# Optimization experiments

Hardware: AMD Instinct MI355X
Metric: run time of the kernel (lower is better)

## Reference

```python
import jax, jax.numpy as jnp
import numpy as np

SEQ = 8192
DIM = 1280
NHEADS = 16
HEAD_DIM = DIM // NHEADS  # 80
NSEG = 8
SEG = SEQ // NSEG  # 1024


def setup_inputs() -> dict:
    key = jax.random.key(0)
    ks = jax.random.split(key, 7)
    hidden_states = jax.random.normal(ks[0], (SEQ, DIM), jnp.float32)
    # realistic rotary embeddings: cos/sin of random angles, shape [S, head_dim]
    ang = jax.random.uniform(ks[1], (SEQ, HEAD_DIM), jnp.float32, 0.0, 2.0 * np.pi)
    cos = jnp.cos(ang)
    sin = jnp.sin(ang)
    qkv_w = jax.random.normal(ks[2], (3 * DIM, DIM), jnp.float32) * (DIM ** -0.5)
    qkv_b = jax.random.normal(ks[3], (3 * DIM,), jnp.float32) * 0.02
    proj_w = jax.random.normal(ks[4], (DIM, DIM), jnp.float32) * (DIM ** -0.5)
    proj_b = jax.random.normal(ks[5], (DIM,), jnp.float32) * 0.02
    cu_seqlens = jnp.arange(NSEG + 1, dtype=jnp.int32) * SEG  # equal segments
    return {"hidden_states": hidden_states, "cos": cos, "sin": sin,
            "qkv_w": qkv_w, "qkv_b": qkv_b, "proj_w": proj_w, "proj_b": proj_b,
            "cu_seqlens": cu_seqlens}


def _rope(x, cos, sin):
    # x: [S, H, D]; cos/sin: [S, D] broadcast over heads. Computed in fp32.
    x = x.astype(jnp.float32)
    d = x.shape[-1]
    x1, x2 = x[..., : d // 2], x[..., d // 2:]
    rot = jnp.concatenate([-x2, x1], axis=-1)
    return x * cos[:, None, :] + rot * sin[:, None, :]


def reference(hidden_states, cos, sin, qkv_w, qkv_b, proj_w, proj_b, cu_seqlens):
    S, dim = hidden_states.shape
    nseg = cu_seqlens.shape[0] - 1
    seg = S // nseg  # segments are equal-length; block-diagonal attention batches over them
    H, D = NHEADS, dim // NHEADS

    qkv = hidden_states @ qkv_w.T + qkv_b                 # [S, 3*dim]
    qkv = qkv.reshape(S, 3, H, D)
    q, k, v = qkv[:, 0], qkv[:, 1], qkv[:, 2]             # [S, H, D]

    in_dtype = hidden_states.dtype
    q = _rope(q, cos, sin).astype(in_dtype)
    k = _rope(k, cos, sin).astype(in_dtype)

    scale = D ** -0.5
    qs = q.reshape(nseg, seg, H, D)
    ks = k.reshape(nseg, seg, H, D)
    vs = v.reshape(nseg, seg, H, D)

    scores = jnp.einsum('bqhd,bkhd->bhqk', qs, ks) * scale  # [nseg, H, seg, seg]
    probs = jax.nn.softmax(scores, axis=-1)
    out = jnp.einsum('bhqk,bkhd->bqhd', probs, vs)          # [nseg, seg, H, D]
    out = out.reshape(S, H * D)
    return out @ proj_w.T + proj_b
```

## Files before the change

kernel.cpp:

```cpp
#include <hip/hip_runtime.h>

#define SEQ 8192
#define DIM 1280
#define NHEADS 16
#define HD 80
#define HDP 96
#define NSEG 8
#define SEG 1024
#define KVB 64
#define NSTEP (SEG / KVB)
#define PST 72

typedef float f32x4 __attribute__((ext_vector_type(4)));
typedef short bf16x8 __attribute__((ext_vector_type(8)));
typedef unsigned int u32;

__device__ __forceinline__ float fast_exp2(float x) {
  return __builtin_amdgcn_exp2f(x);
}

__device__ __forceinline__ short f2bf(float f) {
  unsigned int u = __builtin_bit_cast(unsigned int, f);
  u = (u + 0x7fff + ((u >> 16) & 1)) >> 16;
  return (short)u;
}

__device__ __forceinline__ u32 cvt_pk_bf16(float lo, float hi) {
  u32 r;
  asm("v_cvt_pk_bf16_f32 %0, %1, %2" : "=v"(r) : "v"(lo), "v"(hi));
  return r;
}

typedef __attribute__((address_space(1))) const unsigned int glds_src_t;
typedef __attribute__((address_space(3))) unsigned int glds_dst_t;
__device__ __forceinline__ void gload_lds16(const void* g, void* l) {
  __builtin_amdgcn_global_load_lds((glds_src_t*)g, (glds_dst_t*)l, 16, 0, 0);
}

__global__ void cast_f32_bf16(const float* __restrict__ in, short* __restrict__ out, int n) {
  int n4 = n >> 2;
  for (int i = blockIdx.x * blockDim.x + threadIdx.x; i < n4; i += gridDim.x * blockDim.x) {
    float4 v = ((const float4*)in)[i];
    short4 o;
    o.x = f2bf(v.x); o.y = f2bf(v.y); o.z = f2bf(v.z); o.w = f2bf(v.w);
    ((short4*)out)[i] = o;
  }
}

__global__ __launch_bounds__(256) void gemm_bt_bias(
    const short* __restrict__ A, const short* __restrict__ B,
    const float* __restrict__ bias, float* __restrict__ C,
    int M, int N, int K) {
  __shared__ short As[128 * 64];
  __shared__ short Bs[128 * 64];
  int tid = threadIdx.x;
  int w = tid >> 6, l = tid & 63;
  int lrow = l & 15, lg = l >> 4;
  int bid = blockIdx.x;
  int cpx = gridDim.x >> 3;
  int lid = (bid & 7) * cpx + (bid >> 3);
  int ntx = N >> 7;
  int m0 = (lid / ntx) * 128, n0 = (lid % ntx) * 128;
  int wm = w & 1, wn = w >> 1;

  f32x4 acc[4][4] = {};

  const char* Abase = (const char*)A + (size_t)m0 * K * 2;
  const char* Bbase = (const char*)B + (size_t)n0 * K * 2;

  for (int k0 = 0; k0 < K; k0 += 64) {
#pragma unroll
    for (int j = 0; j < 4; j++) {
      int c = j * 256 + tid;
      int row = c >> 3;
      int sc = c & 7;
      int slc = sc ^ (row & 7);
      size_t goff = (size_t)row * K * 2 + (size_t)k0 * 2 + slc * 16;
      int loff = (j * 256 + w * 64) * 16;
      gload_lds16(Abase + goff, (char*)As + loff);
      gload_lds16(Bbase + goff, (char*)Bs + loff);
    }
    __syncthreads();
#pragma unroll
    for (int kk = 0; kk < 2; kk++) {
      bf16x8 a[4], b[4];
#pragma unroll
      for (int mt = 0; mt < 4; mt++) {
        int row = wm * 64 + mt * 16 + lrow;
        int p = (kk * 4 + lg) ^ (row & 7);
        a[mt] = *(const bf16x8*)&As[row * 64 + p * 8];
      }
#pragma unroll
      for (int nt = 0; nt < 4; nt++) {
        int row = wn * 64 + nt * 16 + lrow;
        int p = (kk * 4 + lg) ^ (row & 7);
        b[nt] = *(const bf16x8*)&Bs[row * 64 + p * 8];
      }
#pragma unroll
      for (int mt = 0; mt < 4; mt++)
#pragma unroll
        for (int nt = 0; nt < 4; nt++)
          acc[mt][nt] = __builtin_amdgcn_mfma_f32_16x16x32_bf16(a[mt], b[nt], acc[mt][nt], 0, 0, 0);
    }
    __syncthreads();
  }
#pragma unroll
  for (int nt = 0; nt < 4; nt++) {
    int col = n0 + wn * 64 + nt * 16 + lrow;
    float bv = bias[col];
#pragma unroll
    for (int mt = 0; mt < 4; mt++) {
      int mrow = m0 + wm * 64 + mt * 16 + lg * 4;
#pragma unroll
      for (int r = 0; r < 4; r++)
        C[(size_t)(mrow + r) * N + col] = acc[mt][nt][r] + bv;
    }
  }
}

__global__ void rope_qk(const float* __restrict__ qkv, const float* __restrict__ cosb,
                        const float* __restrict__ sinb, short* __restrict__ qg,
                        short* __restrict__ kg) {
  int t = blockIdx.x * blockDim.x + threadIdx.x;
  if (t >= SEQ * NHEADS * 40) return;
  int d = t % 40;
  int h = (t / 40) & 15;
  int s = t / 640;
  const float* row = qkv + (size_t)s * (3 * DIM);
  float c0 = cosb[s * HD + d], c1 = cosb[s * HD + d + 40];
  float s0 = sinb[s * HD + d], s1 = sinb[s * HD + d + 40];
  float x1 = row[h * HD + d], x2 = row[h * HD + d + 40];
  float q0 = x1 * c0 - x2 * s0;
  float q1 = x2 * c1 + x1 * s1;
  float y1 = row[DIM + h * HD + d], y2 = row[DIM + h * HD + d + 40];
  float k0 = y1 * c0 - y2 * s0;
  float k1 = y2 * c1 + y1 * s1;
  const float sc = 0.11180339887498949f * 1.4426950408889634f;
  size_t base = ((size_t)h * SEQ + s) * HDP;
  qg[base + d] = f2bf(q0 * sc);
  qg[base + d + 40] = f2bf(q1 * sc);
  kg[base + d] = f2bf(k0);
  kg[base + d + 40] = f2bf(k1);
  if (d < 16) { qg[base + 80 + d] = 0; kg[base + 80 + d] = 0; }
}

__global__ void v_transpose(const float* __restrict__ qkv, short* __restrict__ vt) {
  __shared__ float T[16][68];
  int st = blockIdx.x, dt = blockIdx.y, h = blockIdx.z;
  int d0 = dt * 16, s0 = st * 64;
  int t = threadIdx.x;
  int dd = t & 15, ss = t >> 4;
#pragma unroll
  for (int j = 0; j < 4; j++) {
    int s = ss + j * 16;
    T[dd][s] = qkv[(size_t)(s0 + s) * (3 * DIM) + 2 * DIM + h * HD + d0 + dd];
  }
  __syncthreads();
  int s2 = t & 63, dr = t >> 6;
#pragma unroll
  for (int j = 0; j < 4; j++) {
    int d = dr + j * 4;
    vt[((size_t)(h * HD + d0 + d)) * SEQ + s0 + s2] = f2bf(T[d][s2]);
  }
}

__global__ __launch_bounds__(512, 2) void attn_kernel(
    const short* __restrict__ qg, const short* __restrict__ kg,
    const short* __restrict__ vt, short* __restrict__ out) {
  __shared__ short Ks[2][64 * 128];
  __shared__ short Pl[8][32 * PST];
  int bid = blockIdx.x;
  int b = bid & 7, h = (bid >> 3) & 15, qt = bid >> 7;
  int tid = threadIdx.x;
  int w = tid >> 6, l = tid & 63;
  int lrow = l & 15, lg = l >> 4;
  int qbase_s = b * SEG + qt * 256 + w * 32;

  const short* qh = qg + (size_t)h * SEQ * HDP;
  const short* kh = kg + (size_t)h * SEQ * HDP;
  const short* vh = vt + (size_t)h * HD * SEQ;

#define STAGE_K(BUF, KEY0N)                                                    \
  {                                                                            \
    _Pragma("unroll") for (int sr = 0; sr < 2; sr++) {                         \
      int sbase = sr * 512 + w * 64;                                           \
      int ss = sbase + l;                                                      \
      int skey = ss >> 4, sc = ss & 15;                                        \
      int slc = sc ^ (skey & 7);                                               \
      const short* ssrc =                                                      \
          kh + (size_t)((KEY0N) + skey) * HDP + (slc < 12 ? slc * 8 : 0);      \
      gload_lds16(ssrc, (char*)&Ks[BUF][0] + sbase * 16);                      \
    }                                                                          \
  }

  bf16x8 qf[2][3];
#pragma unroll
  for (int mt = 0; mt < 2; mt++)
#pragma unroll
    for (int ks = 0; ks < 3; ks++)
      qf[mt][ks] = *(const bf16x8*)&qh[(size_t)(qbase_s + mt * 16 + lrow) * HDP + ks * 32 + lg * 8];

  f32x4 o[2][5] = {};
  float m_st[2] = {-1e30f, -1e30f};
  float l_st[2] = {0.f, 0.f};

  short* Pw = &Pl[w][0];

  STAGE_K(0, b * SEG);
  __syncthreads();

  for (int i = 0; i < NSTEP; i++) {
    int cur = i & 1;
    int key0 = b * SEG + i * KVB;
    if (i + 1 < NSTEP) {
      STAGE_K(cur ^ 1, key0 + KVB);
    }

    f32x4 sv[2][4] = {};
    __builtin_amdgcn_s_setprio(1);
#pragma unroll
    for (int kt = 0; kt < 4; kt++) {
      bf16x8 kf[3];
      int key = kt * 16 + lrow;
#pragma unroll
      for (int ks = 0; ks < 3; ks++) {
        int p = (ks * 4 + lg) ^ (key & 7);
        kf[ks] = *(const bf16x8*)&Ks[cur][key * 128 + p * 8];
      }
#pragma unroll
      for (int mt = 0; mt < 2; mt++)
#pragma unroll
        for (int ks = 0; ks < 3; ks++)
          sv[mt][kt] = __builtin_amdgcn_mfma_f32_16x16x32_bf16(kf[ks], qf[mt][ks], sv[mt][kt], 0, 0, 0);
    }
    __builtin_amdgcn_s_setprio(0);

    bf16x8 vf[5][2];
#pragma unroll
    for (int nt = 0; nt < 5; nt++)
#pragma unroll
      for (int ks = 0; ks < 2; ks++)
        vf[nt][ks] = *(const bf16x8*)&vh[(size_t)(nt * 16 + lrow) * SEQ + key0 + ks * 32 + lg * 8];

    float cm[2];
#pragma unroll
    for (int mt = 0; mt < 2; mt++) {
      float a0 = fmaxf(fmaxf(sv[mt][0][0], sv[mt][0][1]), fmaxf(sv[mt][0][2], sv[mt][0][3]));
      float a1 = fmaxf(fmaxf(sv[mt][1][0], sv[mt][1][1]), fmaxf(sv[mt][1][2], sv[mt][1][3]));
      float a2 = fmaxf(fmaxf(sv[mt][2][0], sv[mt][2][1]), fmaxf(sv[mt][2][2], sv[mt][2][3]));
      float a3 = fmaxf(fmaxf(sv[mt][3][0], sv[mt][3][1]), fmaxf(sv[mt][3][2], sv[mt][3][3]));
      float c = fmaxf(fmaxf(a0, a1), fmaxf(a2, a3));
      c = fmaxf(c, __shfl_xor(c, 16));
      c = fmaxf(c, __shfl_xor(c, 32));
      cm[mt] = c;
    }
    if (__any((cm[0] > m_st[0] + 8.f) || (cm[1] > m_st[1] + 8.f))) {
#pragma unroll
      for (int mt = 0; mt < 2; mt++) {
        float mn = fmaxf(m_st[mt], cm[mt]);
        float c = fast_exp2(m_st[mt] - mn);
        m_st[mt] = mn;
        l_st[mt] *= c;
        float cr[4];
#pragma unroll
        for (int r = 0; r < 4; r++) cr[r] = __shfl(c, lg * 4 + r);
#pragma unroll
        for (int nt = 0; nt < 5; nt++)
#pragma unroll
          for (int r = 0; r < 4; r++) o[mt][nt][r] *= cr[r];
      }
    }
#pragma unroll
    for (int mt = 0; mt < 2; mt++) {
      float rs = 0.f;
#pragma unroll
      for (int kt = 0; kt < 4; kt++) {
#pragma unroll
        for (int r = 0; r < 4; r++) {
          sv[mt][kt][r] = fast_exp2(sv[mt][kt][r] - m_st[mt]);
          rs += sv[mt][kt][r];
        }
        uint2 pk;
        pk.x = cvt_pk_bf16(sv[mt][kt][0], sv[mt][kt][1]);
        pk.y = cvt_pk_bf16(sv[mt][kt][2], sv[mt][kt][3]);
        *(uint2*)&Pw[(mt * 16 + lrow) * PST + kt * 16 + lg * 4] = pk;
      }
      rs += __shfl_xor(rs, 16);
      rs += __shfl_xor(rs, 32);
      l_st[mt] += rs;
    }

    bf16x8 pa[2][2];
#pragma unroll
    for (int mt = 0; mt < 2; mt++)
#pragma unroll
      for (int ks = 0; ks < 2; ks++)
        pa[mt][ks] = *(const bf16x8*)&Pw[(mt * 16 + lrow) * PST + ks * 32 + lg * 8];
    __builtin_amdgcn_s_setprio(1);
#pragma unroll
    for (int nt = 0; nt < 5; nt++)
#pragma unroll
      for (int mt = 0; mt < 2; mt++)
#pragma unroll
        for (int ks = 0; ks < 2; ks++)
          o[mt][nt] = __builtin_amdgcn_mfma_f32_16x16x32_bf16(pa[mt][ks], vf[nt][ks], o[mt][nt], 0, 0, 0);
    __builtin_amdgcn_s_setprio(0);

    __syncthreads();
  }

#pragma unroll
  for (int mt = 0; mt < 2; mt++) {
    float rl = 1.f / l_st[mt];
    float ir[4];
#pragma unroll
    for (int r = 0; r < 4; r++) ir[r] = __shfl(rl, lg * 4 + r);
#pragma unroll
    for (int r = 0; r < 4; r++) {
      int srow = qbase_s + mt * 16 + lg * 4 + r;
#pragma unroll
      for (int nt = 0; nt < 5; nt++)
        out[(size_t)srow * DIM + h * HD + nt * 16 + lrow] = f2bf(o[mt][nt][r] * ir[r]);
    }
  }
}

extern "C" void kernel_launch(void* const* d_in, const int* in_sizes, int n_in,
                              void* d_out, int out_size, void* d_ws, size_t ws_size,
                              hipStream_t stream) {
  const float* hidden = (const float*)d_in[0];
  const float* cosb = (const float*)d_in[1];
  const float* sinb = (const float*)d_in[2];
  const float* qkv_w = (const float*)d_in[3];
  const float* qkv_b = (const float*)d_in[4];
  const float* proj_w = (const float*)d_in[5];
  const float* proj_b = (const float*)d_in[6];

  char* ws = (char*)d_ws;
  float* qkv_f = (float*)(ws);
  short* attn_o = (short*)(ws);
  short* wp_bf = (short*)(ws + 23068672);
  short* q_bf = (short*)(ws + 125829120);
  short* k_bf = (short*)(ws + 150994944);
  short* v_tb = (short*)(ws + 176160768);
  short* h_bf = (short*)(ws + 197132288);
  short* wq_bf = (short*)(ws + 218103808);

  cast_f32_bf16<<<4096, 256, 0, stream>>>(hidden, h_bf, SEQ * DIM);
  cast_f32_bf16<<<4096, 256, 0, stream>>>(qkv_w, wq_bf, 3 * DIM * DIM);
  gemm_bt_bias<<<1920, 256, 0, stream>>>(h_bf, wq_bf, qkv_b, qkv_f, SEQ, 3 * DIM, DIM);
  rope_qk<<<20480, 256, 0, stream>>>(qkv_f, cosb, sinb, q_bf, k_bf);
  v_transpose<<<dim3(128, 5, 16), 256, 0, stream>>>(qkv_f, v_tb);
  cast_f32_bf16<<<2048, 256, 0, stream>>>(proj_w, wp_bf, DIM * DIM);
  attn_kernel<<<512, 512, 0, stream>>>(q_bf, k_bf, v_tb, attn_o);
  gemm_bt_bias<<<640, 256, 0, stream>>>(attn_o, wp_bf, proj_b, (float*)d_out, SEQ, DIM, DIM);
}
```

Baseline: 348.7 us.

## Emit bf16 QKV from GEMM and double-buffer GEMM LDS tiles

```diff
diff --git a/kernel.cpp b/kernel.cpp
--- a/kernel.cpp
+++ b/kernel.cpp
@@ -25,6 +25,11 @@
   return (short)u;
 }
 
+__device__ __forceinline__ float bf2f(short s) {
+  u32 u = ((u32)(unsigned short)s) << 16;
+  return __builtin_bit_cast(float, u);
+}
+
 __device__ __forceinline__ u32 cvt_pk_bf16(float lo, float hi) {
   u32 r;
   asm("v_cvt_pk_bf16_f32 %0, %1, %2" : "=v"(r) : "v"(lo), "v"(hi));
@@ -50,9 +55,9 @@
 __global__ __launch_bounds__(256) void gemm_bt_bias(
     const short* __restrict__ A, const short* __restrict__ B,
     const float* __restrict__ bias, float* __restrict__ C,
-    int M, int N, int K) {
-  __shared__ short As[128 * 64];
-  __shared__ short Bs[128 * 64];
+    short* __restrict__ Cb, int M, int N, int K) {
+  __shared__ short As[2][128 * 32];
+  __shared__ short Bs[2][128 * 32];
   int tid = threadIdx.x;
   int w = tid >> 6, l = tid & 63;
   int lrow = l & 15, lg = l >> 4;
@@ -68,42 +73,48 @@
   const char* Abase = (const char*)A + (size_t)m0 * K * 2;
   const char* Bbase = (const char*)B + (size_t)n0 * K * 2;
 
-  for (int k0 = 0; k0 < K; k0 += 64) {
-#pragma unroll
-    for (int j = 0; j < 4; j++) {
-      int c = j * 256 + tid;
-      int row = c >> 3;
-      int sc = c & 7;
-      int slc = sc ^ (row & 7);
-      size_t goff = (size_t)row * K * 2 + (size_t)k0 * 2 + slc * 16;
-      int loff = (j * 256 + w * 64) * 16;
-      gload_lds16(Abase + goff, (char*)As + loff);
-      gload_lds16(Bbase + goff, (char*)Bs + loff);
-    }
+#define STAGE_G(BUF, K0)                                                       \
+  {                                                                            \
+    _Pragma("unroll") for (int j = 0; j < 2; j++) {                            \
+      int c = j * 256 + tid;                                                   \
+      int row = c >> 2;                                                        \
+      int slc = (c & 3) ^ ((row >> 1) & 3);                                    \
+      size_t goff = (size_t)row * K * 2 + (size_t)(K0) * 2 + slc * 16;         \
+      int loff = (j * 256 + w * 64) * 16;                                      \
+      gload_lds16(Abase + goff, (char*)&As[BUF][0] + loff);                    \
+      gload_lds16(Bbase + goff, (char*)&Bs[BUF][0] + loff);                    \
+    }                                                                          \
+  }
+
+  STAGE_G(0, 0);
+  __syncthreads();
+
+  for (int k0 = 0; k0 < K; k0 += 32) {
+    int cur = (k0 >> 5) & 1;
+    if (k0 + 32 < K) {
+      STAGE_G(cur ^ 1, k0 + 32);
+    }
+    bf16x8 a[4], b[4];
+#pragma unroll
+    for (int mt = 0; mt < 4; mt++) {
+      int row = wm * 64 + mt * 16 + lrow;
+      int p = lg ^ ((row >> 1) & 3);
+      a[mt] = *(const bf16x8*)&As[cur][row * 32 + p * 8];
+    }
+#pragma unroll
+    for (int nt = 0; nt < 4; nt++) {
+      int row = wn * 64 + nt * 16 + lrow;
+      int p = lg ^ ((row >> 1) & 3);
+      b[nt] = *(const bf16x8*)&Bs[cur][row * 32 + p * 8];
+    }
+#pragma unroll
+    for (int mt = 0; mt < 4; mt++)
+#pragma unroll
+      for (int nt = 0; nt < 4; nt++)
+        acc[mt][nt] = __builtin_amdgcn_mfma_f32_16x16x32_bf16(a[mt], b[nt], acc[mt][nt], 0, 0, 0);
     __syncthreads();
-#pragma unroll
-    for (int kk = 0; kk < 2; kk++) {
-      bf16x8 a[4], b[4];
-#pragma unroll
-      for (int mt = 0; mt < 4; mt++) {
-        int row = wm * 64 + mt * 16 + lrow;
-        int p = (kk * 4 + lg) ^ (row & 7);
-        a[mt] = *(const bf16x8*)&As[row * 64 + p * 8];
-      }
-#pragma unroll
-      for (int nt = 0; nt < 4; nt++) {
-        int row = wn * 64 + nt * 16 + lrow;
-        int p = (kk * 4 + lg) ^ (row & 7);
-        b[nt] = *(const bf16x8*)&Bs[row * 64 + p * 8];
-      }
-#pragma unroll
-      for (int mt = 0; mt < 4; mt++)
-#pragma unroll
-        for (int nt = 0; nt < 4; nt++)
-          acc[mt][nt] = __builtin_amdgcn_mfma_f32_16x16x32_bf16(a[mt], b[nt], acc[mt][nt], 0, 0, 0);
-    }
-    __syncthreads();
-  }
+  }
+
 #pragma unroll
   for (int nt = 0; nt < 4; nt++) {
     int col = n0 + wn * 64 + nt * 16 + lrow;
@@ -111,14 +122,20 @@
 #pragma unroll
     for (int mt = 0; mt < 4; mt++) {
       int mrow = m0 + wm * 64 + mt * 16 + lg * 4;
-#pragma unroll
-      for (int r = 0; r < 4; r++)
-        C[(size_t)(mrow + r) * N + col] = acc[mt][nt][r] + bv;
-    }
-  }
-}
-
-__global__ void rope_qk(const float* __restrict__ qkv, const float* __restrict__ cosb,
+      if (Cb) {
+#pragma unroll
+        for (int r = 0; r < 4; r++)
+          Cb[(size_t)(mrow + r) * N + col] = f2bf(acc[mt][nt][r] + bv);
+      } else {
+#pragma unroll
+        for (int r = 0; r < 4; r++)
+          C[(size_t)(mrow + r) * N + col] = acc[mt][nt][r] + bv;
+      }
+    }
+  }
+}
+
+__global__ void rope_qk(const short* __restrict__ qkv, const float* __restrict__ cosb,
                         const float* __restrict__ sinb, short* __restrict__ qg,
                         short* __restrict__ kg) {
   int t = blockIdx.x * blockDim.x + threadIdx.x;
@@ -126,13 +143,13 @@
   int d = t % 40;
   int h = (t / 40) & 15;
   int s = t / 640;
-  const float* row = qkv + (size_t)s * (3 * DIM);
+  const short* row = qkv + (size_t)s * (3 * DIM);
   float c0 = cosb[s * HD + d], c1 = cosb[s * HD + d + 40];
   float s0 = sinb[s * HD + d], s1 = sinb[s * HD + d + 40];
-  float x1 = row[h * HD + d], x2 = row[h * HD + d + 40];
+  float x1 = bf2f(row[h * HD + d]), x2 = bf2f(row[h * HD + d + 40]);
   float q0 = x1 * c0 - x2 * s0;
   float q1 = x2 * c1 + x1 * s1;
-  float y1 = row[DIM + h * HD + d], y2 = row[DIM + h * HD + d + 40];
+  float y1 = bf2f(row[DIM + h * HD + d]), y2 = bf2f(row[DIM + h * HD + d + 40]);
   float k0 = y1 * c0 - y2 * s0;
   float k1 = y2 * c1 + y1 * s1;
   const float sc = 0.11180339887498949f * 1.4426950408889634f;
@@ -144,8 +161,8 @@
   if (d < 16) { qg[base + 80 + d] = 0; kg[base + 80 + d] = 0; }
 }
 
-__global__ void v_transpose(const float* __restrict__ qkv, short* __restrict__ vt) {
-  __shared__ float T[16][68];
+__global__ void v_transpose(const short* __restrict__ qkv, short* __restrict__ vt) {
+  __shared__ short T[16][72];
   int st = blockIdx.x, dt = blockIdx.y, h = blockIdx.z;
   int d0 = dt * 16, s0 = st * 64;
   int t = threadIdx.x;
@@ -160,7 +177,7 @@
 #pragma unroll
   for (int j = 0; j < 4; j++) {
     int d = dr + j * 4;
-    vt[((size_t)(h * HD + d0 + d)) * SEQ + s0 + s2] = f2bf(T[d][s2]);
+    vt[((size_t)(h * HD + d0 + d)) * SEQ + s0 + s2] = T[d][s2];
   }
 }
 
@@ -337,7 +354,7 @@
   const float* proj_b = (const float*)d_in[6];
 
   char* ws = (char*)d_ws;
-  float* qkv_f = (float*)(ws);
+  short* qkv_bf = (short*)(ws);
   short* attn_o = (short*)(ws);
   short* wp_bf = (short*)(ws + 23068672);
   short* q_bf = (short*)(ws + 125829120);
@@ -348,10 +365,10 @@
 
   cast_f32_bf16<<<4096, 256, 0, stream>>>(hidden, h_bf, SEQ * DIM);
   cast_f32_bf16<<<4096, 256, 0, stream>>>(qkv_w, wq_bf, 3 * DIM * DIM);
-  gemm_bt_bias<<<1920, 256, 0, stream>>>(h_bf, wq_bf, qkv_b, qkv_f, SEQ, 3 * DIM, DIM);
-  rope_qk<<<20480, 256, 0, stream>>>(qkv_f, cosb, sinb, q_bf, k_bf);
-  v_transpose<<<dim3(128, 5, 16), 256, 0, stream>>>(qkv_f, v_tb);
+  gemm_bt_bias<<<1920, 256, 0, stream>>>(h_bf, wq_bf, qkv_b, nullptr, qkv_bf, SEQ, 3 * DIM, DIM);
+  rope_qk<<<20480, 256, 0, stream>>>(qkv_bf, cosb, sinb, q_bf, k_bf);
+  v_transpose<<<dim3(128, 5, 16), 256, 0, stream>>>(qkv_bf, v_tb);
   cast_f32_bf16<<<2048, 256, 0, stream>>>(proj_w, wp_bf, DIM * DIM);
   attn_kernel<<<512, 512, 0, stream>>>(q_bf, k_bf, v_tb, attn_o);
-  gemm_bt_bias<<<640, 256, 0, stream>>>(attn_o, wp_bf, proj_b, (float*)d_out, SEQ, DIM, DIM);
-}
+  gemm_bt_bias<<<640, 256, 0, stream>>>(attn_o, wp_bf, proj_b, (float*)d_out, nullptr, SEQ, DIM, DIM);
+}
```

Result: faster. 327.0 us (-6.2%).
